# Performance work log

Measured on AMD Instinct MI355X. Metric: run time of the kernel, lower is better.

Reference implementation:

```python
import jax, jax.numpy as jnp
import numpy as np

N_HEADS = 8
TANH_CLIP = 10.0


def setup_inputs() -> dict:
    key = jax.random.key(0)
    ks = jax.random.split(key, 7)
    B, N, D = 128, 1000, 512
    embeddings = jax.random.normal(ks[0], (B, N, D), dtype=jnp.float32)
    step_context = jax.random.normal(ks[1], (B, 1, 2 * D), dtype=jnp.float32)
    # action mask: True = feasible action; guarantee at least one feasible per row
    action_mask = jax.random.uniform(ks[2], (B, 1, N)) > 0.3
    action_mask = action_mask.at[:, :, 0].set(True)
    s = 0.02
    W_node = jax.random.normal(ks[3], (D, 3 * D), dtype=jnp.float32) * s
    W_fixed = jax.random.normal(ks[4], (D, D), dtype=jnp.float32) * s
    W_step = jax.random.normal(ks[5], (2 * D, D), dtype=jnp.float32) * s
    W_out = jax.random.normal(ks[6], (D, D), dtype=jnp.float32) * s
    return {"embeddings": embeddings, "step_context": step_context,
            "action_mask": action_mask, "W_node": W_node, "W_fixed": W_fixed,
            "W_step": W_step, "W_out": W_out}


def reference(embeddings, step_context, action_mask, W_node, W_fixed, W_step, W_out):
    B, N, D = embeddings.shape
    H = N_HEADS
    hd = D // H
    neg_inf = jnp.float32(-jnp.inf)

    # --- precompute (Decoder._precompute) ---
    graph_embed = embeddings.mean(axis=1)                      # [B, D]
    kvl = embeddings @ W_node                                  # [B, N, 3D]
    _gk, gv, logit_key = jnp.split(kvl, 3, axis=-1)
    # source bug: glimpse_key variable is overwritten with glimpse_val, and
    # attention is called with key = value = glimpse_val
    KV = gv.reshape(B, N, H, hd).transpose(0, 2, 1, 3)         # [B, H, N, hd]
    graph_context = (graph_embed @ W_fixed)[:, None, :]        # [B, 1, D]

    # --- per-step query (Decoder._get_log_p) ---
    query = graph_context + step_context @ W_step              # [B, 1, D]
    q = query.reshape(B, 1, H, hd).transpose(0, 2, 1, 3)       # [B, H, 1, hd]

    # --- inner MHA (scaled_dot_product_attention with boolean mask) ---
    scores = jnp.einsum('bhqs,bhns->bhqn', q, KV) / jnp.sqrt(jnp.float32(hd))
    scores = jnp.where(action_mask[:, None, :, :], scores, neg_inf)  # [B,H,1,N]
    attn = jax.nn.softmax(scores, axis=-1)
    heads = jnp.einsum('bhqn,bhns->bhqs', attn, KV)            # [B, H, 1, hd]
    heads = heads.transpose(0, 2, 1, 3).reshape(B, 1, D)       # [B, 1, D]

    # --- glimpse projection and logit head ---
    glimpse = heads @ W_out                                    # [B, 1, D]
    logits = jnp.einsum('bqd,bnd->bqn', glimpse, logit_key) / jnp.sqrt(jnp.float32(D))
    logits = jnp.tanh(logits) * TANH_CLIP
    logits = jnp.where(action_mask, logits, neg_inf)
    return jax.nn.log_softmax(logits, axis=-1)                 # [B, 1, N]
```

## Files before the change

kernel.cpp:

```cpp
#include <hip/hip_runtime.h>
#include <math.h>

#define B 128
#define N 1000
#define D 512
#define H 8
#define NCH 10
#define CHK 100
#define NCHM 25
#define CHKM 40

#define OFF_QW    0
#define OFF_PMEAN (OFF_QW + B*H*D)
#define OFF_PAE   OFF_PMEAN
#define OFF_ZC    (OFF_PAE + B*NCH*H*D)
#define OFF_GW    (OFF_ZC + B*NCH*H)
#define OFF_LG    (OFF_GW + B*D)
#define OFF_LMAX  (OFF_LG + B*N)
#define OFF_LSUM  (OFF_LMAX + B*NCH)

__device__ inline float dot4(float4 a, float4 b){
    float r = a.x * b.x;
    r = fmaf(a.y, b.y, r);
    r = fmaf(a.z, b.z, r);
    r = fmaf(a.w, b.w, r);
    return r;
}

__global__ void k1_partial_mean(const float* __restrict__ emb, float* __restrict__ ws){
    int chunk = blockIdx.x, b = blockIdx.y, t = threadIdx.x;
    const float4* e4 = (const float4*)emb + ((size_t)b * N + (size_t)chunk * CHKM) * (D / 4) + t;
    float4 a0 = make_float4(0,0,0,0), a1 = a0, a2 = a0, a3 = a0;
    for (int n = 0; n < CHKM; n += 4) {
        float4 v0 = e4[(size_t)(n + 0) * (D / 4)];
        float4 v1 = e4[(size_t)(n + 1) * (D / 4)];
        float4 v2 = e4[(size_t)(n + 2) * (D / 4)];
        float4 v3 = e4[(size_t)(n + 3) * (D / 4)];
        a0.x += v0.x; a0.y += v0.y; a0.z += v0.z; a0.w += v0.w;
        a1.x += v1.x; a1.y += v1.y; a1.z += v1.z; a1.w += v1.w;
        a2.x += v2.x; a2.y += v2.y; a2.z += v2.z; a2.w += v2.w;
        a3.x += v3.x; a3.y += v3.y; a3.z += v3.z; a3.w += v3.w;
    }
    float4 acc;
    acc.x = (a0.x + a1.x) + (a2.x + a3.x);
    acc.y = (a0.y + a1.y) + (a2.y + a3.y);
    acc.z = (a0.z + a1.z) + (a2.z + a3.z);
    acc.w = (a0.w + a1.w) + (a2.w + a3.w);
    ((float4*)(ws + OFF_PMEAN + (size_t)(b * NCHM + chunk) * D))[t] = acc;
}

__global__ void k2_prep(const float* __restrict__ stepc, const float* __restrict__ Wnode,
                        const float* __restrict__ Wfix, const float* __restrict__ Wstep,
                        float* __restrict__ ws){
    int b = blockIdx.x, d = threadIdx.x;
    __shared__ float ge[D];
    __shared__ float q[D];
    float s = 0.f;
    #pragma unroll
    for (int c = 0; c < NCHM; ++c) s += ws[OFF_PMEAN + (size_t)(b * NCHM + c) * D + d];
    ge[d] = s * (1.0f / N);
    __syncthreads();
    float a0 = 0.f, a1 = 0.f, a2 = 0.f, a3 = 0.f;
    for (int k = 0; k < D; k += 4) {
        a0 = fmaf(ge[k],     Wfix[(size_t)k * D + d],       a0);
        a1 = fmaf(ge[k + 1], Wfix[(size_t)(k + 1) * D + d], a1);
        a2 = fmaf(ge[k + 2], Wfix[(size_t)(k + 2) * D + d], a2);
        a3 = fmaf(ge[k + 3], Wfix[(size_t)(k + 3) * D + d], a3);
    }
    const float* sc = stepc + (size_t)b * 2 * D;
    for (int k = 0; k < 2 * D; k += 4) {
        a0 = fmaf(sc[k],     Wstep[(size_t)k * D + d],       a0);
        a1 = fmaf(sc[k + 1], Wstep[(size_t)(k + 1) * D + d], a1);
        a2 = fmaf(sc[k + 2], Wstep[(size_t)(k + 2) * D + d], a2);
        a3 = fmaf(sc[k + 3], Wstep[(size_t)(k + 3) * D + d], a3);
    }
    q[d] = (a0 + a1) + (a2 + a3);
    __syncthreads();
    const float* wrow = Wnode + (size_t)d * 3 * D + D;
    #pragma unroll
    for (int h = 0; h < H; ++h) {
        float a = 0.f;
        const float* qh = q + h * 64;
        const float* wh = wrow + h * 64;
        #pragma unroll 8
        for (int s2 = 0; s2 < 64; ++s2) a = fmaf(qh[s2], wh[s2], a);
        ws[OFF_QW + ((size_t)b * H + h) * D + d] = a;
    }
}

__global__ __launch_bounds__(256, 4) void kb_attn(const float* __restrict__ emb,
        const unsigned char* __restrict__ mask, float* __restrict__ ws){
    const int cg = blockIdx.x, b = blockIdx.y, t = threadIdx.x;
    const int w = t >> 6, l = t & 63;
    __shared__ float p_lds[CHK][H];
    float4 qlo[H], qhi[H];
    {
        const float* qb = ws + OFF_QW + (size_t)b * H * D;
        #pragma unroll
        for (int h = 0; h < H; ++h) {
            qlo[h] = *(const float4*)(qb + (size_t)h * D + 4 * l);
            qhi[h] = *(const float4*)(qb + (size_t)h * D + 256 + 4 * l);
        }
    }
    const float* embb = emb + ((size_t)b * N + (size_t)cg * CHK) * D;
    const unsigned char* mb = mask + (size_t)b * N + cg * CHK;
    for (int i = 0; i < CHK / 4; ++i) {
        const int nl = 4 * i + w;
        const float4* er = (const float4*)(embb + (size_t)nl * D) + l;
        float4 e0 = er[0];
        float4 e1 = er[64];
        float s[H];
        #pragma unroll
        for (int h = 0; h < H; ++h)
            s[h] = dot4(e0, qlo[h]) + dot4(e1, qhi[h]);
        #pragma unroll
        for (int o = 32; o > 0; o >>= 1) {
            #pragma unroll
            for (int h = 0; h < H; ++h) s[h] += __shfl_xor(s[h], o);
        }
        if (l == 0) {
            bool m = mb[nl] != 0;
            float4 p0, p1;
            p0.x = m ? __expf(s[0] * 0.125f) : 0.f;
            p0.y = m ? __expf(s[1] * 0.125f) : 0.f;
            p0.z = m ? __expf(s[2] * 0.125f) : 0.f;
            p0.w = m ? __expf(s[3] * 0.125f) : 0.f;
            p1.x = m ? __expf(s[4] * 0.125f) : 0.f;
            p1.y = m ? __expf(s[5] * 0.125f) : 0.f;
            p1.z = m ? __expf(s[6] * 0.125f) : 0.f;
            p1.w = m ? __expf(s[7] * 0.125f) : 0.f;
            *(float4*)&p_lds[nl][0] = p0;
            *(float4*)&p_lds[nl][4] = p1;
        }
    }
    __syncthreads();
    if (t < H) {
        float z = 0.f;
        for (int i = 0; i < CHK; ++i) z += p_lds[i][t];
        ws[OFF_ZC + ((size_t)b * NCH + cg) * H + t] = z;
    }
    {
        float2 acc[H];
        #pragma unroll
        for (int h = 0; h < H; ++h) acc[h] = make_float2(0.f, 0.f);
        const float2* ecol = (const float2*)embb + t;
        #pragma unroll 2
        for (int i = 0; i < CHK; ++i) {
            float2 e = ecol[(size_t)i * (D / 2)];
            float4 pa = *(const float4*)&p_lds[i][0];
            float4 pb = *(const float4*)&p_lds[i][4];
            acc[0].x = fmaf(pa.x, e.x, acc[0].x); acc[0].y = fmaf(pa.x, e.y, acc[0].y);
            acc[1].x = fmaf(pa.y, e.x, acc[1].x); acc[1].y = fmaf(pa.y, e.y, acc[1].y);
            acc[2].x = fmaf(pa.z, e.x, acc[2].x); acc[2].y = fmaf(pa.z, e.y, acc[2].y);
            acc[3].x = fmaf(pa.w, e.x, acc[3].x); acc[3].y = fmaf(pa.w, e.y, acc[3].y);
            acc[4].x = fmaf(pb.x, e.x, acc[4].x); acc[4].y = fmaf(pb.x, e.y, acc[4].y);
            acc[5].x = fmaf(pb.y, e.x, acc[5].x); acc[5].y = fmaf(pb.y, e.y, acc[5].y);
            acc[6].x = fmaf(pb.z, e.x, acc[6].x); acc[6].y = fmaf(pb.z, e.y, acc[6].y);
            acc[7].x = fmaf(pb.w, e.x, acc[7].x); acc[7].y = fmaf(pb.w, e.y, acc[7].y);
        }
        float2* paeb = (float2*)(ws + OFF_PAE) + ((size_t)(b * NCH + cg) * H) * (D / 2) + t;
        #pragma unroll
        for (int h = 0; h < H; ++h) paeb[(size_t)h * (D / 2)] = acc[h];
    }
}

__global__ __launch_bounds__(512) void kd_post(const float* __restrict__ Wnode,
        const float* __restrict__ Wout, float* __restrict__ ws){
    int b = blockIdx.x, t = threadIdx.x;
    __shared__ float ae[H * D];
    __shared__ float heads[D];
    __shared__ float gl[D];
    __shared__ float iZ[H];
    if (t < H) {
        float Z = 0.f;
        #pragma unroll
        for (int c = 0; c < NCH; ++c)
            Z += ws[OFF_ZC + ((size_t)b * NCH + c) * H + t];
        iZ[t] = 1.0f / Z;
    }
    __syncthreads();
    #pragma unroll
    for (int h = 0; h < H; ++h) {
        float s = 0.f;
        #pragma unroll
        for (int c = 0; c < NCH; ++c)
            s += ws[OFF_PAE + (((size_t)b * NCH + c) * H + h) * (size_t)D + t];
        ae[h * D + t] = s * iZ[h];
    }
    __syncthreads();
    {
        int h = t >> 6;
        const float* aeh = ae + h * D;
        const float* col = Wnode + 512 + t;
        float a0 = 0.f, a1 = 0.f, a2 = 0.f, a3 = 0.f;
        for (int d = 0; d < D; d += 4) {
            a0 = fmaf(aeh[d],     col[(size_t)d * (3 * D)],       a0);
            a1 = fmaf(aeh[d + 1], col[(size_t)(d + 1) * (3 * D)], a1);
            a2 = fmaf(aeh[d + 2], col[(size_t)(d + 2) * (3 * D)], a2);
            a3 = fmaf(aeh[d + 3], col[(size_t)(d + 3) * (3 * D)], a3);
        }
        heads[t] = (a0 + a1) + (a2 + a3);
    }
    __syncthreads();
    {
        float a0 = 0.f, a1 = 0.f, a2 = 0.f, a3 = 0.f;
        for (int d = 0; d < D; d += 4) {
            a0 = fmaf(heads[d],     Wout[(size_t)d * D + t],       a0);
            a1 = fmaf(heads[d + 1], Wout[(size_t)(d + 1) * D + t], a1);
            a2 = fmaf(heads[d + 2], Wout[(size_t)(d + 2) * D + t], a2);
            a3 = fmaf(heads[d + 3], Wout[(size_t)(d + 3) * D + t], a3);
        }
        gl[t] = (a0 + a1) + (a2 + a3);
    }
    __syncthreads();
    {
        const float* wrow = Wnode + (size_t)t * (3 * D) + 2 * D;
        float a0 = 0.f, a1 = 0.f, a2 = 0.f, a3 = 0.f;
        for (int e = 0; e < D; e += 4) {
            a0 = fmaf(gl[e],     wrow[e],     a0);
            a1 = fmaf(gl[e + 1], wrow[e + 1], a1);
            a2 = fmaf(gl[e + 2], wrow[e + 2], a2);
            a3 = fmaf(gl[e + 3], wrow[e + 3], a3);
        }
        ws[OFF_GW + (size_t)b * D + t] = (a0 + a1) + (a2 + a3);
    }
}

__global__ __launch_bounds__(256, 4) void kc_logits(const float* __restrict__ emb,
        const unsigned char* __restrict__ mask, float* __restrict__ ws){
    const int cg = blockIdx.x, b = blockIdx.y, t = threadIdx.x;
    const int w = t >> 6, l = t & 63;
    __shared__ float wm[4], wsum[4];
    float4 glo, ghi;
    {
        const float* gb = ws + OFF_GW + (size_t)b * D;
        glo = *(const float4*)(gb + 4 * l);
        ghi = *(const float4*)(gb + 256 + 4 * l);
    }
    const float* embb = emb + ((size_t)b * N + (size_t)cg * CHK) * D;
    const unsigned char* mb = mask + (size_t)b * N + cg * CHK;
    float m = -INFINITY, s = 0.f;
    for (int i = 0; i < CHK / 4; ++i) {
        const int nl = 4 * i + w;
        const float4* er = (const float4*)(embb + (size_t)nl * D) + l;
        float4 e0 = er[0];
        float4 e1 = er[64];
        float a = dot4(e0, glo) + dot4(e1, ghi);
        #pragma unroll
        for (int o = 32; o > 0; o >>= 1) a += __shfl_xor(a, o);
        bool mk = mb[nl] != 0;
        float lg = mk ? tanhf(a * 0.044194173824159216f) * 10.0f : -INFINITY;
        if (l == 0) ws[OFF_LG + (size_t)b * N + cg * CHK + nl] = lg;
        if (mk) {
            float mn = fmaxf(m, lg);
            s = s * __expf(m - mn) + __expf(lg - mn);
            m = mn;
        }
    }
    if (l == 0) { wm[w] = m; wsum[w] = s; }
    __syncthreads();
    if (t == 0) {
        float M = -INFINITY;
        #pragma unroll
        for (int i = 0; i < 4; ++i) M = fmaxf(M, wm[i]);
        float S = 0.f;
        #pragma unroll
        for (int i = 0; i < 4; ++i)
            if (wm[i] != -INFINITY) S += wsum[i] * __expf(wm[i] - M);
        ws[OFF_LMAX + (size_t)b * NCH + cg] = M;
        ws[OFF_LSUM + (size_t)b * NCH + cg] = S;
    }
}

__global__ void k8_out(const float* __restrict__ ws, float* __restrict__ out){
    int b = blockIdx.x, t = threadIdx.x;
    __shared__ float Ls;
    if (t == 0) {
        float M = -INFINITY;
        #pragma unroll
        for (int c = 0; c < NCH; ++c)
            M = fmaxf(M, ws[OFF_LMAX + (size_t)b * NCH + c]);
        float S = 0.f;
        #pragma unroll
        for (int c = 0; c < NCH; ++c) {
            float m = ws[OFF_LMAX + (size_t)b * NCH + c];
            if (m != -INFINITY) S += __expf(m - M) * ws[OFF_LSUM + (size_t)b * NCH + c];
        }
        Ls = M + __logf(S);
    }
    __syncthreads();
    float L = Ls;
    for (int j = t; j < N; j += 256)
        out[(size_t)b * N + j] = fmaxf(ws[OFF_LG + (size_t)b * N + j] - L, -1e30f);
}

extern "C" void kernel_launch(void* const* d_in, const int* in_sizes, int n_in,
                              void* d_out, int out_size, void* d_ws, size_t ws_size,
                              hipStream_t stream) {
    const float* emb   = (const float*)d_in[0];
    const float* stepc = (const float*)d_in[1];
    const unsigned char* mask = (const unsigned char*)d_in[2];
    const float* Wnode = (const float*)d_in[3];
    const float* Wfix  = (const float*)d_in[4];
    const float* Wstep = (const float*)d_in[5];
    const float* Wout  = (const float*)d_in[6];
    float* out = (float*)d_out;
    float* ws  = (float*)d_ws;

    k1_partial_mean<<<dim3(NCHM, B), 128, 0, stream>>>(emb, ws);
    k2_prep<<<dim3(B), 512, 0, stream>>>(stepc, Wnode, Wfix, Wstep, ws);
    kb_attn<<<dim3(NCH, B), 256, 0, stream>>>(emb, mask, ws);
    kd_post<<<dim3(B), 512, 0, stream>>>(Wnode, Wout, ws);
    kc_logits<<<dim3(NCH, B), 256, 0, stream>>>(emb, mask, ws);
    k8_out<<<dim3(B), 256, 0, stream>>>(ws, out);
}
```

Baseline: 363.4 us.

## Split attention kernel into score and PV kernels with partial shuffle reductions

Splits the fused attention kernel into a score kernel and a separate P·V kernel. The exp weights pass through a new workspace buffer, and the PAE region no longer aliases the partial means. Score reduction now stops at 16-lane groups and finishes in shared memory, where all threads apply the mask and exp and accumulate Z with shared atomics. Occupancy hints are dropped from launch bounds. The aim is to cut serial shuffle and single-lane exp work, at the cost of one extra launch and an extra pass reading the embedding chunk.

```diff
diff --git a/kernel.cpp b/kernel.cpp
--- a/kernel.cpp
+++ b/kernel.cpp
@@ -12,8 +12,9 @@
 
 #define OFF_QW    0
 #define OFF_PMEAN (OFF_QW + B*H*D)
-#define OFF_PAE   OFF_PMEAN
-#define OFF_ZC    (OFF_PAE + B*NCH*H*D)
+#define OFF_PAE   (OFF_PMEAN + B*NCHM*D)
+#define OFF_P     (OFF_PAE + B*NCH*H*D)
+#define OFF_ZC    (OFF_P + B*N*H)
 #define OFF_GW    (OFF_ZC + B*NCH*H)
 #define OFF_LG    (OFF_GW + B*D)
 #define OFF_LMAX  (OFF_LG + B*N)
@@ -88,11 +89,13 @@
     }
 }
 
-__global__ __launch_bounds__(256, 4) void kb_attn(const float* __restrict__ emb,
+__global__ __launch_bounds__(256) void kb_scores(const float* __restrict__ emb,
         const unsigned char* __restrict__ mask, float* __restrict__ ws){
     const int cg = blockIdx.x, b = blockIdx.y, t = threadIdx.x;
-    const int w = t >> 6, l = t & 63;
-    __shared__ float p_lds[CHK][H];
+    const int w = t >> 6, l = t & 63, g = l >> 4;
+    __shared__ float part[CHK][4][H];
+    __shared__ float zsh[H];
+    if (t < H) zsh[t] = 0.f;
     float4 qlo[H], qhi[H];
     {
         const float* qb = ws + OFF_QW + (size_t)b * H * D;
@@ -103,7 +106,6 @@
         }
     }
     const float* embb = emb + ((size_t)b * N + (size_t)cg * CHK) * D;
-    const unsigned char* mb = mask + (size_t)b * N + cg * CHK;
     for (int i = 0; i < CHK / 4; ++i) {
         const int nl = 4 * i + w;
         const float4* er = (const float4*)(embb + (size_t)nl * D) + l;
@@ -114,54 +116,61 @@
         for (int h = 0; h < H; ++h)
             s[h] = dot4(e0, qlo[h]) + dot4(e1, qhi[h]);
         #pragma unroll
-        for (int o = 32; o > 0; o >>= 1) {
+        for (int o = 1; o <= 8; o <<= 1) {
             #pragma unroll
             for (int h = 0; h < H; ++h) s[h] += __shfl_xor(s[h], o);
         }
-        if (l == 0) {
-            bool m = mb[nl] != 0;
-            float4 p0, p1;
-            p0.x = m ? __expf(s[0] * 0.125f) : 0.f;
-            p0.y = m ? __expf(s[1] * 0.125f) : 0.f;
-            p0.z = m ? __expf(s[2] * 0.125f) : 0.f;
-            p0.w = m ? __expf(s[3] * 0.125f) : 0.f;
-            p1.x = m ? __expf(s[4] * 0.125f) : 0.f;
-            p1.y = m ? __expf(s[5] * 0.125f) : 0.f;
-            p1.z = m ? __expf(s[6] * 0.125f) : 0.f;
-            p1.w = m ? __expf(s[7] * 0.125f) : 0.f;
-            *(float4*)&p_lds[nl][0] = p0;
-            *(float4*)&p_lds[nl][4] = p1;
-        }
-    }
-    __syncthreads();
-    if (t < H) {
-        float z = 0.f;
-        for (int i = 0; i < CHK; ++i) z += p_lds[i][t];
-        ws[OFF_ZC + ((size_t)b * NCH + cg) * H + t] = z;
-    }
-    {
-        float2 acc[H];
-        #pragma unroll
-        for (int h = 0; h < H; ++h) acc[h] = make_float2(0.f, 0.f);
-        const float2* ecol = (const float2*)embb + t;
-        #pragma unroll 2
-        for (int i = 0; i < CHK; ++i) {
-            float2 e = ecol[(size_t)i * (D / 2)];
-            float4 pa = *(const float4*)&p_lds[i][0];
-            float4 pb = *(const float4*)&p_lds[i][4];
-            acc[0].x = fmaf(pa.x, e.x, acc[0].x); acc[0].y = fmaf(pa.x, e.y, acc[0].y);
-            acc[1].x = fmaf(pa.y, e.x, acc[1].x); acc[1].y = fmaf(pa.y, e.y, acc[1].y);
-            acc[2].x = fmaf(pa.z, e.x, acc[2].x); acc[2].y = fmaf(pa.z, e.y, acc[2].y);
-            acc[3].x = fmaf(pa.w, e.x, acc[3].x); acc[3].y = fmaf(pa.w, e.y, acc[3].y);
-            acc[4].x = fmaf(pb.x, e.x, acc[4].x); acc[4].y = fmaf(pb.x, e.y, acc[4].y);
-            acc[5].x = fmaf(pb.y, e.x, acc[5].x); acc[5].y = fmaf(pb.y, e.y, acc[5].y);
-            acc[6].x = fmaf(pb.z, e.x, acc[6].x); acc[6].y = fmaf(pb.z, e.y, acc[6].y);
-            acc[7].x = fmaf(pb.w, e.x, acc[7].x); acc[7].y = fmaf(pb.w, e.y, acc[7].y);
-        }
-        float2* paeb = (float2*)(ws + OFF_PAE) + ((size_t)(b * NCH + cg) * H) * (D / 2) + t;
-        #pragma unroll
-        for (int h = 0; h < H; ++h) paeb[(size_t)h * (D / 2)] = acc[h];
-    }
+        if ((l & 15) == 0) {
+            *(float4*)&part[nl][g][0] = make_float4(s[0], s[1], s[2], s[3]);
+            *(float4*)&part[nl][g][4] = make_float4(s[4], s[5], s[6], s[7]);
+        }
+    }
+    __syncthreads();
+    const unsigned char* mb = mask + (size_t)b * N + cg * CHK;
+    float* pout = ws + OFF_P + ((size_t)b * N + (size_t)cg * CHK) * H;
+    for (int slot = t; slot < CHK * H; slot += 256) {
+        int r = slot >> 3, h = slot & 7;
+        float v = (part[r][0][h] + part[r][1][h]) + (part[r][2][h] + part[r][3][h]);
+        bool m = mb[r] != 0;
+        float pe = m ? __expf(v * 0.125f) : 0.f;
+        pout[slot] = pe;
+        atomicAdd(&zsh[h], pe);
+    }
+    __syncthreads();
+    if (t < H) ws[OFF_ZC + ((size_t)b * NCH + cg) * H + t] = zsh[t];
+}
+
+__global__ __launch_bounds__(256) void kb_pv(const float* __restrict__ emb,
+        float* __restrict__ ws){
+    const int cg = blockIdx.x, b = blockIdx.y, t = threadIdx.x;
+    __shared__ float p_lds[CHK][H];
+    {
+        const float* pin = ws + OFF_P + ((size_t)b * N + (size_t)cg * CHK) * H;
+        for (int s = t; s < CHK * H; s += 256) ((float*)p_lds)[s] = pin[s];
+    }
+    __syncthreads();
+    const float* embb = emb + ((size_t)b * N + (size_t)cg * CHK) * D;
+    float2 acc[H];
+    #pragma unroll
+    for (int h = 0; h < H; ++h) acc[h] = make_float2(0.f, 0.f);
+    const float2* ecol = (const float2*)embb + t;
+    #pragma unroll 2
+    for (int i = 0; i < CHK; ++i) {
+        float2 e = ecol[(size_t)i * (D / 2)];
+        float4 pa = *(const float4*)&p_lds[i][0];
+        float4 pb = *(const float4*)&p_lds[i][4];
+        acc[0].x = fmaf(pa.x, e.x, acc[0].x); acc[0].y = fmaf(pa.x, e.y, acc[0].y);
+        acc[1].x = fmaf(pa.y, e.x, acc[1].x); acc[1].y = fmaf(pa.y, e.y, acc[1].y);
+        acc[2].x = fmaf(pa.z, e.x, acc[2].x); acc[2].y = fmaf(pa.z, e.y, acc[2].y);
+        acc[3].x = fmaf(pa.w, e.x, acc[3].x); acc[3].y = fmaf(pa.w, e.y, acc[3].y);
+        acc[4].x = fmaf(pb.x, e.x, acc[4].x); acc[4].y = fmaf(pb.x, e.y, acc[4].y);
+        acc[5].x = fmaf(pb.y, e.x, acc[5].x); acc[5].y = fmaf(pb.y, e.y, acc[5].y);
+        acc[6].x = fmaf(pb.z, e.x, acc[6].x); acc[6].y = fmaf(pb.z, e.y, acc[6].y);
+        acc[7].x = fmaf(pb.w, e.x, acc[7].x); acc[7].y = fmaf(pb.w, e.y, acc[7].y);
+    }
+    float2* paeb = (float2*)(ws + OFF_PAE) + ((size_t)(b * NCH + cg) * H) * (D / 2) + t;
+    #pragma unroll
+    for (int h = 0; h < H; ++h) paeb[(size_t)h * (D / 2)] = acc[h];
 }
 
 __global__ __launch_bounds__(512) void kd_post(const float* __restrict__ Wnode,
@@ -226,7 +235,7 @@
     }
 }
 
-__global__ __launch_bounds__(256, 4) void kc_logits(const float* __restrict__ emb,
+__global__ __launch_bounds__(256) void kc_logits(const float* __restrict__ emb,
         const unsigned char* __restrict__ mask, float* __restrict__ ws){
     const int cg = blockIdx.x, b = blockIdx.y, t = threadIdx.x;
     const int w = t >> 6, l = t & 63;
@@ -309,7 +318,8 @@
 
     k1_partial_mean<<<dim3(NCHM, B), 128, 0, stream>>>(emb, ws);
     k2_prep<<<dim3(B), 512, 0, stream>>>(stepc, Wnode, Wfix, Wstep, ws);
-    kb_attn<<<dim3(NCH, B), 256, 0, stream>>>(emb, mask, ws);
+    kb_scores<<<dim3(NCH, B), 256, 0, stream>>>(emb, mask, ws);
+    kb_pv<<<dim3(NCH, B), 256, 0, stream>>>(emb, ws);
     kd_post<<<dim3(B), 512, 0, stream>>>(Wnode, Wout, ws);
     kc_logits<<<dim3(NCH, B), 256, 0, stream>>>(emb, mask, ws);
     k8_out<<<dim3(B), 256, 0, stream>>>(ws, out);
```

Result: no change. 366.8 us (+0.9%).
